# Optimization experiments

Hardware: AMD Instinct MI355X
Metric: run time of the kernel (lower is better)

## Reference

```python
import jax, jax.numpy as jnp
import numpy as np

S, E, CAP = 4096, 64, 128


def setup_inputs() -> dict:
    key = jax.random.key(0)
    k1, k2 = jax.random.split(key)
    logits = jax.random.normal(k1, (S, E), dtype=jnp.float32)
    noise = jax.random.normal(k2, (S, E), dtype=jnp.float32)
    return {"logits": logits, "noise": noise, "capacity": CAP}


def reference(logits, noise, capacity):
    # logits, noise: [S, E]; capacity: python int
    gates = jax.nn.softmax(logits, axis=1)                      # [S, E]
    num_experts = gates.shape[1]

    # top-1 expert
    indices1_s = jnp.argmax(gates, axis=1)                      # [S]
    mask1 = jax.nn.one_hot(indices1_s, num_experts, dtype=jnp.int32)

    # top-2 expert from noised logits with top-1 masked out
    logits_w_noise = logits + noise
    neg_min = jnp.finfo(logits.dtype).min
    logits_except1 = jnp.where(mask1 > 0, neg_min, logits_w_noise)
    indices2_s = jnp.argmax(logits_except1, axis=1)
    mask2 = jax.nn.one_hot(indices2_s, num_experts, dtype=jnp.int32)

    # capacity locations (running count per expert over tokens)
    locations1 = jnp.cumsum(mask1, axis=0) - 1                  # [S, E]
    locations2 = jnp.cumsum(mask2, axis=0) - 1
    locations2 = locations2 + jnp.sum(mask1, axis=0, keepdims=True)

    # load-balancing aux loss
    me = jnp.mean(gates, axis=0)
    ce = jnp.mean(mask1.astype(logits.dtype), axis=0)
    l_aux = jnp.mean(me * ce) * num_experts * num_experts

    # drop tokens over capacity
    mask1 = mask1 * (locations1 < capacity).astype(mask1.dtype)
    mask2 = mask2 * (locations2 < capacity).astype(mask2.dtype)

    locations1_s = jnp.sum(locations1 * mask1, axis=1)          # [S]
    locations2_s = jnp.sum(locations2 * mask2, axis=1)

    mask1_f = mask1.astype(logits.dtype)
    mask2_f = mask2.astype(logits.dtype)
    gates1_s = jnp.einsum('se,se->s', gates, mask1_f)
    gates2_s = jnp.einsum('se,se->s', gates, mask2_f)
    denom_s = jnp.maximum(gates1_s + gates2_s, jnp.finfo(logits.dtype).eps)
    gates1_s = gates1_s / denom_s
    gates2_s = gates2_s / denom_s

    gates1 = gates1_s[:, None] * mask1_f                        # [S, E]
    gates2 = gates2_s[:, None] * mask2_f

    locations1_sc = jax.nn.one_hot(locations1_s, capacity, dtype=logits.dtype)
    locations2_sc = jax.nn.one_hot(locations2_s, capacity, dtype=logits.dtype)

    combine_weights = (gates1[:, :, None] * locations1_sc[:, None, :]
                       + gates2[:, :, None] * locations2_sc[:, None, :])  # [S, E, C]
    dispatch_mask = combine_weights.astype(bool)
    return l_aux, combine_weights, dispatch_mask
```

## Files before the change

### kernel.cpp

```cpp
#include <hip/hip_runtime.h>
#include <float.h>
#include <math.h>

#define SS 4096
#define EE 64
#define CAPC 128
#define SEC (4096LL * 64 * 128)

__global__ __launch_bounds__(256) void zero_out_kernel(float4* __restrict__ out4,
                                                       long n4,
                                                       float* __restrict__ tail,
                                                       int ntail,
                                                       float* __restrict__ gate_sums) {
    long i = (long)blockIdx.x * blockDim.x + threadIdx.x;
    long stride = (long)gridDim.x * blockDim.x;
    float4 z = make_float4(0.f, 0.f, 0.f, 0.f);
    for (; i < n4; i += stride) out4[i] = z;
    if (blockIdx.x == 0) {
        if (threadIdx.x < 64) gate_sums[threadIdx.x] = 0.f;
        if ((int)threadIdx.x < ntail) tail[threadIdx.x] = 0.f;
    }
}

__global__ __launch_bounds__(256) void gate_kernel(const float* __restrict__ logits,
                                                   const float* __restrict__ noise,
                                                   int* __restrict__ idx1s,
                                                   int* __restrict__ idx2s,
                                                   float* __restrict__ g1raw,
                                                   float* __restrict__ g2raw,
                                                   float* __restrict__ gate_sums) {
    const int tid  = threadIdx.x;
    const int wave = tid >> 6;
    const int lane = tid & 63;
    const int s    = blockIdx.x * 4 + wave;

    const float l = logits[s * EE + lane];
    const float n = noise[s * EE + lane];

    float v = l; int bi = lane;
    #pragma unroll
    for (int off = 32; off; off >>= 1) {
        float v2 = __shfl_xor(v, off, 64);
        int   i2 = __shfl_xor(bi, off, 64);
        if (v2 > v || (v2 == v && i2 < bi)) { v = v2; bi = i2; }
    }
    const int idx1 = bi;
    const float m = v;

    float e = expf(l - m);
    float sum = e;
    #pragma unroll
    for (int off = 32; off; off >>= 1) sum += __shfl_xor(sum, off, 64);
    const float gate = e / sum;
    const float g1 = __shfl(gate, idx1, 64);

    float lw = (lane == idx1) ? -FLT_MAX : (l + n);
    float v2v = lw; int bi2 = lane;
    #pragma unroll
    for (int off = 32; off; off >>= 1) {
        float v2 = __shfl_xor(v2v, off, 64);
        int   i2 = __shfl_xor(bi2, off, 64);
        if (v2 > v2v || (v2 == v2v && i2 < bi2)) { v2v = v2; bi2 = i2; }
    }
    const int idx2 = bi2;
    const float g2 = __shfl(gate, idx2, 64);

    if (lane == 0) {
        idx1s[s] = idx1;
        idx2s[s] = idx2;
        g1raw[s] = g1;
        g2raw[s] = g2;
    }

    __shared__ float sg[256];
    sg[tid] = gate;
    __syncthreads();
    if (tid < 64) {
        float t = sg[tid] + sg[tid + 64] + sg[tid + 128] + sg[tid + 192];
        atomicAdd(&gate_sums[tid], t);
    }
}

__global__ __launch_bounds__(64) void chunk_rank_kernel(const int* __restrict__ idx1s,
                                                        const int* __restrict__ idx2s,
                                                        int* __restrict__ wrank1,
                                                        int* __restrict__ wrank2,
                                                        int* __restrict__ cnt1,
                                                        int* __restrict__ cnt2) {
    __shared__ int li1[64], li2[64];
    const int t = threadIdx.x;
    const int chunk = blockIdx.x;
    const int s = chunk * 64 + t;
    li1[t] = idx1s[s];
    li2[t] = idx2s[s];
    __syncthreads();
    const int my1 = li1[t], my2 = li2[t];
    int r1 = 0, r2 = 0, c1 = 0, c2 = 0;
    #pragma unroll 8
    for (int j = 0; j < 64; ++j) {
        const int a = li1[j], b = li2[j];
        r1 += (int)((j < t) & (a == my1));
        r2 += (int)((j < t) & (b == my2));
        c1 += (int)(a == t);
        c2 += (int)(b == t);
    }
    wrank1[s] = r1;
    wrank2[s] = r2;
    cnt1[chunk * 64 + t] = c1;
    cnt2[chunk * 64 + t] = c2;
}

__global__ __launch_bounds__(64) void scan_kernel(const int* __restrict__ cnt1,
                                                  const int* __restrict__ cnt2,
                                                  int* __restrict__ off1,
                                                  int* __restrict__ off2,
                                                  int* __restrict__ count1,
                                                  const float* __restrict__ gate_sums,
                                                  float* __restrict__ d_out) {
    const int e = threadIdx.x;
    int o1 = 0, o2 = 0;
    #pragma unroll 8
    for (int c = 0; c < 64; ++c) {
        off1[c * 64 + e] = o1; o1 += cnt1[c * 64 + e];
        off2[c * 64 + e] = o2; o2 += cnt2[c * 64 + e];
    }
    count1[e] = o1;

    float prod = gate_sums[e] * (float)o1;
    #pragma unroll
    for (int off = 32; off; off >>= 1) prod += __shfl_xor(prod, off, 64);
    if (e == 0) {
        d_out[0] = prod * (float)EE / ((float)SS * (float)SS);
    }
}

__global__ __launch_bounds__(256) void scatter_kernel(const int* __restrict__ idx1s,
                                                      const int* __restrict__ idx2s,
                                                      const int* __restrict__ wrank1,
                                                      const int* __restrict__ wrank2,
                                                      const int* __restrict__ off1,
                                                      const int* __restrict__ off2,
                                                      const int* __restrict__ count1,
                                                      const float* __restrict__ g1raw,
                                                      const float* __restrict__ g2raw,
                                                      float* __restrict__ d_out) {
    const int s = blockIdx.x * 256 + threadIdx.x;
    if (s >= SS) return;
    const int i1 = idx1s[s];
    const int i2 = idx2s[s];
    const int chunk = s >> 6;
    const int loc1 = wrank1[s] + off1[chunk * 64 + i1];
    const int loc2 = wrank2[s] + off2[chunk * 64 + i2] + count1[i2];
    float g1 = g1raw[s];
    float g2 = g2raw[s];
    const bool k1 = loc1 < CAPC;
    const bool k2 = loc2 < CAPC;
    g1 = k1 ? g1 : 0.f;
    g2 = k2 ? g2 : 0.f;
    const float denom = fmaxf(g1 + g2, 1.1920929e-07f);
    g1 /= denom;
    g2 /= denom;

    float* combine = d_out + 1;
    float* mask    = d_out + 1 + SEC;
    const long base = (long)s * (EE * CAPC);
    if (k1 && g1 != 0.f) {
        const long p = base + (long)i1 * CAPC + loc1;
        combine[p] = g1;
        mask[p]    = 1.f;
    }
    if (k2 && g2 != 0.f) {
        const long p = base + (long)i2 * CAPC + loc2;
        combine[p] = g2;
        mask[p]    = 1.f;
    }
}

extern "C" void kernel_launch(void* const* d_in, const int* in_sizes, int n_in,
                              void* d_out, int out_size, void* d_ws, size_t ws_size,
                              hipStream_t stream) {
    const float* logits = (const float*)d_in[0];
    const float* noise  = (const float*)d_in[1];
    float* out = (float*)d_out;

    char* ws = (char*)d_ws;
    int*   idx1s     = (int*)  (ws + 0);
    int*   idx2s     = (int*)  (ws + 16384);
    int*   wrank1    = (int*)  (ws + 32768);
    int*   wrank2    = (int*)  (ws + 49152);
    float* g1raw     = (float*)(ws + 65536);
    float* g2raw     = (float*)(ws + 81920);
    int*   cnt1      = (int*)  (ws + 98304);
    int*   cnt2      = (int*)  (ws + 114688);
    int*   off1      = (int*)  (ws + 131072);
    int*   off2      = (int*)  (ws + 147456);
    int*   count1    = (int*)  (ws + 163840);
    float* gate_sums = (float*)(ws + 164096);

    const long n4 = (long)out_size / 4;
    const int ntail = (int)((long)out_size - n4 * 4);

    zero_out_kernel<<<4096, 256, 0, stream>>>((float4*)out, n4, out + n4 * 4, ntail, gate_sums);
    gate_kernel<<<SS / 4, 256, 0, stream>>>(logits, noise, idx1s, idx2s, g1raw, g2raw, gate_sums);
    chunk_rank_kernel<<<64, 64, 0, stream>>>(idx1s, idx2s, wrank1, wrank2, cnt1, cnt2);
    scan_kernel<<<1, 64, 0, stream>>>(cnt1, cnt2, off1, off2, count1, gate_sums, out);
    scatter_kernel<<<SS / 256, 256, 0, stream>>>(idx1s, idx2s, wrank1, wrank2,
                                                 off1, off2, count1, g1raw, g2raw, out);
}
```

Baseline: 303.8 us.

## Fuse output zeroing with scatter and replace gate-sum atomics with partial reductions

Removes the separate full-output zeroing kernel. Each scatter block now zeroes the combine and mask rows for its four tokens, syncs, then writes its nonzero entries. This drops one launch and a pass over the output. Per-block gate sums go to a partial buffer that the rank and scan kernels reduce, instead of using atomics, and l_aux is staged in workspace and written by the fused kernel. Each block writing a contiguous region may change DRAM write efficiency.

```diff
diff --git a/kernel.cpp b/kernel.cpp
--- a/kernel.cpp
+++ b/kernel.cpp
@@ -5,22 +5,8 @@
 #define SS 4096
 #define EE 64
 #define CAPC 128
+#define ROW (EE * CAPC)
 #define SEC (4096LL * 64 * 128)
-
-__global__ __launch_bounds__(256) void zero_out_kernel(float4* __restrict__ out4,
-                                                       long n4,
-                                                       float* __restrict__ tail,
-                                                       int ntail,
-                                                       float* __restrict__ gate_sums) {
-    long i = (long)blockIdx.x * blockDim.x + threadIdx.x;
-    long stride = (long)gridDim.x * blockDim.x;
-    float4 z = make_float4(0.f, 0.f, 0.f, 0.f);
-    for (; i < n4; i += stride) out4[i] = z;
-    if (blockIdx.x == 0) {
-        if (threadIdx.x < 64) gate_sums[threadIdx.x] = 0.f;
-        if ((int)threadIdx.x < ntail) tail[threadIdx.x] = 0.f;
-    }
-}
 
 __global__ __launch_bounds__(256) void gate_kernel(const float* __restrict__ logits,
                                                    const float* __restrict__ noise,
@@ -28,7 +14,7 @@
                                                    int* __restrict__ idx2s,
                                                    float* __restrict__ g1raw,
                                                    float* __restrict__ g2raw,
-                                                   float* __restrict__ gate_sums) {
+                                                   float* __restrict__ partial) {
     const int tid  = threadIdx.x;
     const int wave = tid >> 6;
     const int lane = tid & 63;
@@ -76,23 +62,31 @@
     sg[tid] = gate;
     __syncthreads();
     if (tid < 64) {
-        float t = sg[tid] + sg[tid + 64] + sg[tid + 128] + sg[tid + 192];
-        atomicAdd(&gate_sums[tid], t);
-    }
-}
-
-__global__ __launch_bounds__(64) void chunk_rank_kernel(const int* __restrict__ idx1s,
-                                                        const int* __restrict__ idx2s,
-                                                        int* __restrict__ wrank1,
-                                                        int* __restrict__ wrank2,
-                                                        int* __restrict__ cnt1,
-                                                        int* __restrict__ cnt2) {
+        partial[blockIdx.x * 64 + tid] =
+            sg[tid] + sg[tid + 64] + sg[tid + 128] + sg[tid + 192];
+    }
+}
+
+__global__ __launch_bounds__(64) void rank_kernel(const int* __restrict__ idx1s,
+                                                  const int* __restrict__ idx2s,
+                                                  int* __restrict__ wrank1,
+                                                  int* __restrict__ wrank2,
+                                                  int* __restrict__ cnt1,
+                                                  int* __restrict__ cnt2,
+                                                  const float* __restrict__ partial,
+                                                  float* __restrict__ partial2) {
     __shared__ int li1[64], li2[64];
     const int t = threadIdx.x;
     const int chunk = blockIdx.x;
     const int s = chunk * 64 + t;
     li1[t] = idx1s[s];
     li2[t] = idx2s[s];
+
+    float acc = 0.f;
+    #pragma unroll
+    for (int k = 0; k < 16; ++k) acc += partial[(chunk * 16 + k) * 64 + t];
+    partial2[chunk * 64 + t] = acc;
+
     __syncthreads();
     const int my1 = li1[t], my2 = li2[t];
     int r1 = 0, r2 = 0, c1 = 0, c2 = 0;
@@ -115,8 +109,8 @@
                                                   int* __restrict__ off1,
                                                   int* __restrict__ off2,
                                                   int* __restrict__ count1,
-                                                  const float* __restrict__ gate_sums,
-                                                  float* __restrict__ d_out) {
+                                                  const float* __restrict__ partial2,
+                                                  float* __restrict__ laux_ws) {
     const int e = threadIdx.x;
     int o1 = 0, o2 = 0;
     #pragma unroll 8
@@ -126,53 +120,88 @@
     }
     count1[e] = o1;
 
-    float prod = gate_sums[e] * (float)o1;
+    float gs = 0.f;
+    #pragma unroll 8
+    for (int c = 0; c < 64; ++c) gs += partial2[c * 64 + e];
+
+    float prod = gs * (float)o1;
     #pragma unroll
     for (int off = 32; off; off >>= 1) prod += __shfl_xor(prod, off, 64);
     if (e == 0) {
-        d_out[0] = prod * (float)EE / ((float)SS * (float)SS);
-    }
-}
-
-__global__ __launch_bounds__(256) void scatter_kernel(const int* __restrict__ idx1s,
-                                                      const int* __restrict__ idx2s,
-                                                      const int* __restrict__ wrank1,
-                                                      const int* __restrict__ wrank2,
-                                                      const int* __restrict__ off1,
-                                                      const int* __restrict__ off2,
-                                                      const int* __restrict__ count1,
-                                                      const float* __restrict__ g1raw,
-                                                      const float* __restrict__ g2raw,
-                                                      float* __restrict__ d_out) {
-    const int s = blockIdx.x * 256 + threadIdx.x;
-    if (s >= SS) return;
-    const int i1 = idx1s[s];
-    const int i2 = idx2s[s];
-    const int chunk = s >> 6;
-    const int loc1 = wrank1[s] + off1[chunk * 64 + i1];
-    const int loc2 = wrank2[s] + off2[chunk * 64 + i2] + count1[i2];
-    float g1 = g1raw[s];
-    float g2 = g2raw[s];
-    const bool k1 = loc1 < CAPC;
-    const bool k2 = loc2 < CAPC;
-    g1 = k1 ? g1 : 0.f;
-    g2 = k2 ? g2 : 0.f;
-    const float denom = fmaxf(g1 + g2, 1.1920929e-07f);
-    g1 /= denom;
-    g2 /= denom;
-
-    float* combine = d_out + 1;
-    float* mask    = d_out + 1 + SEC;
-    const long base = (long)s * (EE * CAPC);
-    if (k1 && g1 != 0.f) {
-        const long p = base + (long)i1 * CAPC + loc1;
-        combine[p] = g1;
-        mask[p]    = 1.f;
-    }
-    if (k2 && g2 != 0.f) {
-        const long p = base + (long)i2 * CAPC + loc2;
-        combine[p] = g2;
-        mask[p]    = 1.f;
+        laux_ws[0] = prod * (float)EE / ((float)SS * (float)SS);
+    }
+}
+
+__global__ __launch_bounds__(256) void zero_scatter_kernel(const int* __restrict__ idx1s,
+                                                           const int* __restrict__ idx2s,
+                                                           const int* __restrict__ wrank1,
+                                                           const int* __restrict__ wrank2,
+                                                           const int* __restrict__ off1,
+                                                           const int* __restrict__ off2,
+                                                           const int* __restrict__ count1,
+                                                           const float* __restrict__ g1raw,
+                                                           const float* __restrict__ g2raw,
+                                                           const float* __restrict__ laux_ws,
+                                                           float* __restrict__ out) {
+    const int tid = threadIdx.x;
+    const int t0  = blockIdx.x * 4;
+    const long cb = (long)t0 * ROW;
+
+    int i1 = 0, i2 = 0, loc1 = 0, loc2 = 0;
+    float g1 = 0.f, g2 = 0.f;
+    bool k1 = false, k2 = false;
+    if (tid < 4) {
+        const int s = t0 + tid;
+        i1 = idx1s[s];
+        i2 = idx2s[s];
+        const int chunk = s >> 6;
+        loc1 = wrank1[s] + off1[chunk * 64 + i1];
+        loc2 = wrank2[s] + off2[chunk * 64 + i2] + count1[i2];
+        g1 = g1raw[s];
+        g2 = g2raw[s];
+        k1 = loc1 < CAPC;
+        k2 = loc2 < CAPC;
+        g1 = k1 ? g1 : 0.f;
+        g2 = k2 ? g2 : 0.f;
+        const float denom = fmaxf(g1 + g2, 1.1920929e-07f);
+        g1 /= denom;
+        g2 /= denom;
+    }
+
+    const float4 z = make_float4(0.f, 0.f, 0.f, 0.f);
+    float4* p4 = (float4*)(out + cb + 4);
+    float4* q4 = (float4*)(out + SEC + cb + 4);
+    #pragma unroll
+    for (int i = tid; i < 8191; i += 256) p4[i] = z;
+    #pragma unroll
+    for (int i = tid; i < 8191; i += 256) q4[i] = z;
+    if (tid < 3) {
+        out[cb + 1 + tid] = 0.f;
+        out[SEC + cb + 1 + tid] = 0.f;
+    } else if (tid == 3) {
+        out[cb + 4L * ROW] = 0.f;
+        out[SEC + cb + 4L * ROW] = 0.f;
+    }
+    __syncthreads();
+
+    if (tid < 4) {
+        const int s = t0 + tid;
+        float* combine = out + 1;
+        float* mask    = out + 1 + SEC;
+        const long base = (long)s * ROW;
+        if (k1 && g1 != 0.f) {
+            const long p = base + (long)i1 * CAPC + loc1;
+            combine[p] = g1;
+            mask[p]    = 1.f;
+        }
+        if (k2 && g2 != 0.f) {
+            const long p = base + (long)i2 * CAPC + loc2;
+            combine[p] = g2;
+            mask[p]    = 1.f;
+        }
+    }
+    if (tid == 4 && blockIdx.x == 0) {
+        out[0] = laux_ws[0];
     }
 }
 
@@ -184,26 +213,25 @@
     float* out = (float*)d_out;
 
     char* ws = (char*)d_ws;
-    int*   idx1s     = (int*)  (ws + 0);
-    int*   idx2s     = (int*)  (ws + 16384);
-    int*   wrank1    = (int*)  (ws + 32768);
-    int*   wrank2    = (int*)  (ws + 49152);
-    float* g1raw     = (float*)(ws + 65536);
-    float* g2raw     = (float*)(ws + 81920);
-    int*   cnt1      = (int*)  (ws + 98304);
-    int*   cnt2      = (int*)  (ws + 114688);
-    int*   off1      = (int*)  (ws + 131072);
-    int*   off2      = (int*)  (ws + 147456);
-    int*   count1    = (int*)  (ws + 163840);
-    float* gate_sums = (float*)(ws + 164096);
-
-    const long n4 = (long)out_size / 4;
-    const int ntail = (int)((long)out_size - n4 * 4);
-
-    zero_out_kernel<<<4096, 256, 0, stream>>>((float4*)out, n4, out + n4 * 4, ntail, gate_sums);
-    gate_kernel<<<SS / 4, 256, 0, stream>>>(logits, noise, idx1s, idx2s, g1raw, g2raw, gate_sums);
-    chunk_rank_kernel<<<64, 64, 0, stream>>>(idx1s, idx2s, wrank1, wrank2, cnt1, cnt2);
-    scan_kernel<<<1, 64, 0, stream>>>(cnt1, cnt2, off1, off2, count1, gate_sums, out);
-    scatter_kernel<<<SS / 256, 256, 0, stream>>>(idx1s, idx2s, wrank1, wrank2,
-                                                 off1, off2, count1, g1raw, g2raw, out);
-}
+    int*   idx1s    = (int*)  (ws + 0);
+    int*   idx2s    = (int*)  (ws + 16384);
+    int*   wrank1   = (int*)  (ws + 32768);
+    int*   wrank2   = (int*)  (ws + 49152);
+    float* g1raw    = (float*)(ws + 65536);
+    float* g2raw    = (float*)(ws + 81920);
+    int*   cnt1     = (int*)  (ws + 98304);
+    int*   cnt2     = (int*)  (ws + 114688);
+    int*   off1     = (int*)  (ws + 131072);
+    int*   off2     = (int*)  (ws + 147456);
+    int*   count1   = (int*)  (ws + 163840);
+    float* laux_ws  = (float*)(ws + 164352);
+    float* partial  = (float*)(ws + 196608);
+    float* partial2 = (float*)(ws + 458752);
+
+    gate_kernel<<<SS / 4, 256, 0, stream>>>(logits, noise, idx1s, idx2s, g1raw, g2raw, partial);
+    rank_kernel<<<64, 64, 0, stream>>>(idx1s, idx2s, wrank1, wrank2, cnt1, cnt2, partial, partial2);
+    scan_kernel<<<1, 64, 0, stream>>>(cnt1, cnt2, off1, off2, count1, partial2, laux_ws);
+    zero_scatter_kernel<<<SS / 4, 256, 0, stream>>>(idx1s, idx2s, wrank1, wrank2,
+                                                    off1, off2, count1, g1raw, g2raw,
+                                                    laux_ws, out);
+}
```

New measurement: 284.9 us. -6.2%, faster.
